# Kernel optimization log

Hardware: AMD Instinct MI355X
Metric: run time of the kernel (lower is better)

The kernel has to match this reference:

```python
import jax, jax.numpy as jnp
import numpy as np

B, S, D, H, HD = 1, 2048, 1024, 16, 64
WINDOW = 512
RADIUS = max(1, WINDOW // 2)
GLOBAL_IDX = (0, 1, 2, 3)
NEG = -1e9


def rotate_half(x):
    x1, x2 = jnp.split(x, 2, axis=-1)
    return jnp.concatenate([-x2, x1], axis=-1)


def apply_rope(x, cos, sin, pos):
    # x: [b, s, h, hd]; cos/sin: [max_pos, hd]; pos: [b, s]
    c = cos[pos][:, :, None, :]
    s_ = sin[pos][:, :, None, :]
    return x * c + rotate_half(x) * s_


def setup_inputs() -> dict:
    key = jax.random.key(0)
    ks = jax.random.split(key, 12)
    x = jax.random.normal(ks[0], (B, S, D), dtype=jnp.float32)
    # RoPE tables (standard construction)
    inv_freq = 1.0 / (10000.0 ** (jnp.arange(0, HD, 2, dtype=jnp.float32) / HD))
    t = jnp.arange(S, dtype=jnp.float32)
    freqs = jnp.outer(t, inv_freq)                      # [S, HD/2]
    emb = jnp.concatenate([freqs, freqs], axis=-1)      # [S, HD]
    cos_freqs = jnp.cos(emb)
    sin_freqs = jnp.sin(emb)
    position_ids = jnp.broadcast_to(jnp.arange(S, dtype=jnp.int32), (B, S))
    w = lambda k: jax.random.normal(k, (D, D), dtype=jnp.float32) * 0.02
    return {
        "x": x, "cos_freqs": cos_freqs, "sin_freqs": sin_freqs,
        "position_ids": position_ids,
        "Wqs": w(ks[1]), "Wks": w(ks[2]), "Wvs": w(ks[3]),
        "Wqg": w(ks[4]), "Wkg": w(ks[5]), "Wvg": w(ks[6]),
        "Wo": w(ks[7]),
    }


def reference(x, cos_freqs, sin_freqs, position_ids, Wqs, Wks, Wvs, Wqg, Wkg, Wvg, Wo):
    b, s, d = x.shape
    split = lambda y: y.reshape(b, s, H, HD)
    qs = split(x @ Wqs)
    ks_ = split(x @ Wks)
    vs = split(x @ Wvs)
    kg = split(x @ Wkg)
    vg = split(x @ Wvg)
    # (qg projection exists in the module but is unused by its forward math)
    qs = apply_rope(qs, cos_freqs, sin_freqs, position_ids)
    ks_ = apply_rope(ks_, cos_freqs, sin_freqs, position_ids)

    qs_t = jnp.swapaxes(qs, 1, 2)   # [b,h,s,hd]
    ks_t = jnp.swapaxes(ks_, 1, 2)
    vs_t = jnp.swapaxes(vs, 1, 2)
    scale = 1.0 / jnp.sqrt(jnp.float32(HD))

    # local sliding-window (causal) attention over dense scores
    scores = jnp.einsum('bhsd,bhtd->bhst', qs_t, ks_t) * scale
    i = jnp.arange(s)[:, None]
    j = jnp.arange(s)[None, :]
    mask = (jnp.abs(i - j) <= RADIUS) & (j <= i)
    scores = jnp.where(mask[None, None], scores, NEG)
    g = jnp.array(GLOBAL_IDX)
    scores = scores.at[:, :, :, g].add(1e9)  # same as per-index set(score+1e9)
    attn = jax.nn.softmax(scores, axis=-1)
    out_local = jnp.einsum('bhst,bhtd->bhsd', attn, vs_t)
    out_local = jnp.swapaxes(out_local, 1, 2).reshape(b, s, d)

    # global attention: all queries attend to the global-index columns of kg/vg
    kg_t = jnp.swapaxes(kg, 1, 2)
    vg_t = jnp.swapaxes(vg, 1, 2)
    scores_g = jnp.einsum('bhsd,bhtd->bhst', qs_t, kg_t) * scale
    col_mask = jnp.zeros((s,), dtype=bool).at[g].set(True)
    scores_g = jnp.where(col_mask[None, None, None, :], scores_g, NEG)
    attn_g = jax.nn.softmax(scores_g, axis=-1)
    out_global = jnp.einsum('bhst,bhtd->bhsd', attn_g, vg_t)
    out_global = jnp.swapaxes(out_global, 1, 2).reshape(b, s, d)

    return (out_local + out_global) @ Wo
```

## Files before the change

kernel.cpp:

```cpp
#include <hip/hip_runtime.h>

typedef _Float16 half8 __attribute__((ext_vector_type(8)));
typedef float floatx4 __attribute__((ext_vector_type(4)));

#define SEQ 2048
#define DMODEL 1024
#define NHEADS 16
#define HEADDIM 64
#define PW 5120

__global__ __launch_bounds__(256) void k_prep(
    const float* __restrict__ x,
    const float* __restrict__ w0, const float* __restrict__ w1, const float* __restrict__ w2,
    const float* __restrict__ w3, const float* __restrict__ w4, const float* __restrict__ w5,
    _Float16* __restrict__ xh, _Float16* __restrict__ wcat, _Float16* __restrict__ wot) {
  const int tid = threadIdx.x;
  const int b = blockIdx.x;
  if (b < 1024) {
    int base = b * 2048 + tid * 8;
    floatx4 f0 = *(const floatx4*)(x + base);
    floatx4 f1 = *(const floatx4*)(x + base + 4);
    half8 h;
    #pragma unroll
    for (int e = 0; e < 4; ++e) { h[e] = (_Float16)f0[e]; h[e + 4] = (_Float16)f1[e]; }
    *(half8*)(xh + base) = h;
    return;
  }
  __shared__ _Float16 T[64][72];
  int t = b - 1024;
  int z = t >> 8;
  int tile = t & 255;
  int k0 = (tile >> 4) * 64, n0 = (tile & 15) * 64;
  const float* W = (z == 0) ? w0 : (z == 1) ? w1 : (z == 2) ? w2
                 : (z == 3) ? w3 : (z == 4) ? w4 : w5;
  _Float16* dst = (z < 5) ? (wcat + (size_t)z * 1024 * 1024) : wot;

  int lr = tid >> 2, c0 = (tid & 3) * 16;
  #pragma unroll
  for (int i = 0; i < 4; ++i) {
    floatx4 f = *(const floatx4*)(W + (size_t)(k0 + lr) * DMODEL + n0 + c0 + i * 4);
    #pragma unroll
    for (int e = 0; e < 4; ++e) T[c0 + i * 4 + e][lr] = (_Float16)f[e];
  }
  __syncthreads();
  int nr = tid >> 2, s0 = (tid & 3) * 16;
  #pragma unroll
  for (int i = 0; i < 2; ++i) {
    half8 h = *(const half8*)&T[nr][s0 + i * 8];
    *(half8*)(dst + (size_t)(n0 + nr) * DMODEL + k0 + s0 + i * 8) = h;
  }
}

template <bool HALF_OUT, bool FUSE_ROPE>
__global__ __launch_bounds__(256) void k_gemm128(const _Float16* __restrict__ A,
                                                 const _Float16* __restrict__ Bt,
                                                 void* __restrict__ Cv,
                                                 const float* __restrict__ cos_t,
                                                 const float* __restrict__ sin_t,
                                                 const int* __restrict__ pos,
                                                 int M, int N, int K) {
  __shared__ _Float16 As[128][64];
  __shared__ _Float16 Bs[128][64];
  const int tid = threadIdx.x;
  const int lane = tid & 63;
  const int w = tid >> 6;
  const int wm = (w >> 1) * 64;
  const int wn = (w & 1) * 64;
  const int l15 = lane & 15;
  const int q4 = lane >> 4;
  const int m0 = blockIdx.x * 128;
  const int n0 = blockIdx.y * 128;

  floatx4 acc[4][4];
  #pragma unroll
  for (int i = 0; i < 4; ++i)
    #pragma unroll
    for (int j = 0; j < 4; ++j) acc[i][j] = (floatx4){0.f, 0.f, 0.f, 0.f};

  _Float16* asBase = &As[0][0];
  _Float16* bsBase = &Bs[0][0];
  const int swz = l15 & 7;

  for (int k0 = 0; k0 < K; k0 += 64) {
    __syncthreads();
    #pragma unroll
    for (int it = 0; it < 4; ++it) {
      int c = it * 256 + tid;
      int r = c >> 3, cc = c & 7;
      int g = cc ^ (r & 7);
      __builtin_amdgcn_global_load_lds(
          (const __attribute__((address_space(1))) void*)(A + (size_t)(m0 + r) * K + k0 + g * 8),
          (__attribute__((address_space(3))) void*)(asBase + (it * 256 + w * 64) * 8),
          16, 0, 0);
      __builtin_amdgcn_global_load_lds(
          (const __attribute__((address_space(1))) void*)(Bt + (size_t)(n0 + r) * K + k0 + g * 8),
          (__attribute__((address_space(3))) void*)(bsBase + (it * 256 + w * 64) * 8),
          16, 0, 0);
    }
    __syncthreads();

    #pragma unroll
    for (int kk = 0; kk < 2; ++kk) {
      int q = kk * 4 + q4;
      half8 af[4], bf[4];
      #pragma unroll
      for (int t = 0; t < 4; ++t) {
        int ar = wm + t * 16 + l15;
        af[t] = *(const half8*)(asBase + (size_t)ar * 64 + ((q ^ swz) * 8));
        int br = wn + t * 16 + l15;
        bf[t] = *(const half8*)(bsBase + (size_t)br * 64 + ((q ^ swz) * 8));
      }
      #pragma unroll
      for (int i = 0; i < 4; ++i)
        #pragma unroll
        for (int j = 0; j < 4; ++j)
          acc[i][j] = __builtin_amdgcn_mfma_f32_16x16x32_f16(af[i], bf[j], acc[i][j], 0, 0, 0);
    }
  }

  #pragma unroll
  for (int tm = 0; tm < 4; ++tm) {
    #pragma unroll
    for (int r = 0; r < 4; ++r) {
      int row = m0 + wm + tm * 16 + q4 * 4 + r;
      float v[4];
      #pragma unroll
      for (int tn = 0; tn < 4; ++tn) v[tn] = acc[tm][tn][r];
      if (FUSE_ROPE && n0 < 2048) {
        int p = pos[row];
        #pragma unroll
        for (int tn = 0; tn < 2; ++tn) {
          int d = tn * 16 + l15;
          float a = acc[tm][tn][r];
          float bvv = acc[tm][tn + 2][r];
          float c1 = cos_t[p * 64 + d],      s1 = sin_t[p * 64 + d];
          float c2 = cos_t[p * 64 + d + 32], s2 = sin_t[p * 64 + d + 32];
          v[tn]     = a * c1 - bvv * s1;
          v[tn + 2] = bvv * c2 + a * s2;
        }
      }
      #pragma unroll
      for (int tn = 0; tn < 4; ++tn) {
        int col = n0 + wn + tn * 16 + l15;
        if (HALF_OUT)
          ((_Float16*)Cv)[(size_t)row * N + col] = (_Float16)v[tn];
        else
          ((float*)Cv)[(size_t)row * N + col] = v[tn];
      }
    }
  }
}

template <bool HALF_OUT>
__global__ __launch_bounds__(256) void k_gemm(const _Float16* __restrict__ A,
                                              const _Float16* __restrict__ Bt,
                                              void* __restrict__ Cv, int M, int N, int K) {
  __shared__ _Float16 As[64][72];
  __shared__ _Float16 Bs[64][72];
  const int tid = threadIdx.x;
  const int lane = tid & 63;
  const int wave = tid >> 6;
  const int wm = (wave >> 1) * 32;
  const int wn = (wave & 1) * 32;
  const int row16 = lane & 15;
  const int q4 = lane >> 4;
  const int m0 = blockIdx.x * 64;
  const int n0 = blockIdx.y * 64;

  floatx4 acc[2][2];
  #pragma unroll
  for (int a = 0; a < 2; ++a)
    #pragma unroll
    for (int b = 0; b < 2; ++b) acc[a][b] = (floatx4){0.f, 0.f, 0.f, 0.f};

  for (int k0 = 0; k0 < K; k0 += 64) {
    __syncthreads();
    #pragma unroll
    for (int rep = 0; rep < 2; ++rep) {
      int c = tid + rep * 256;
      int r = c >> 3, q = c & 7;
      *(half8*)&As[r][q * 8] = *(const half8*)(A + (size_t)(m0 + r) * K + k0 + q * 8);
      *(half8*)&Bs[r][q * 8] = *(const half8*)(Bt + (size_t)(n0 + r) * K + k0 + q * 8);
    }
    __syncthreads();
    #pragma unroll
    for (int kk = 0; kk < 64; kk += 32) {
      half8 a0 = *(const half8*)&As[wm + row16][kk + q4 * 8];
      half8 a1 = *(const half8*)&As[wm + 16 + row16][kk + q4 * 8];
      half8 b0 = *(const half8*)&Bs[wn + row16][kk + q4 * 8];
      half8 b1 = *(const half8*)&Bs[wn + 16 + row16][kk + q4 * 8];
      acc[0][0] = __builtin_amdgcn_mfma_f32_16x16x32_f16(a0, b0, acc[0][0], 0, 0, 0);
      acc[0][1] = __builtin_amdgcn_mfma_f32_16x16x32_f16(a0, b1, acc[0][1], 0, 0, 0);
      acc[1][0] = __builtin_amdgcn_mfma_f32_16x16x32_f16(a1, b0, acc[1][0], 0, 0, 0);
      acc[1][1] = __builtin_amdgcn_mfma_f32_16x16x32_f16(a1, b1, acc[1][1], 0, 0, 0);
    }
  }
  #pragma unroll
  for (int im = 0; im < 2; ++im)
    #pragma unroll
    for (int in = 0; in < 2; ++in)
      #pragma unroll
      for (int r = 0; r < 4; ++r) {
        int row = m0 + wm + im * 16 + q4 * 4 + r;
        int col = n0 + wn + in * 16 + row16;
        if (HALF_OUT)
          ((_Float16*)Cv)[(size_t)row * N + col] = (_Float16)acc[im][in][r];
        else
          ((float*)Cv)[(size_t)row * N + col] = acc[im][in][r];
      }
}

__global__ __launch_bounds__(256, 4) void k_attn(const _Float16* __restrict__ proj,
                                                 _Float16* __restrict__ out) {
  const int tid = threadIdx.x;
  const int hb = blockIdx.y * 64;

  if (blockIdx.x >= 28) {
    const int i = (blockIdx.x - 28) * 4 + (tid >> 6);
    const int lane = tid & 63;
    const float scale = 0.125f;
    float qv = (float)proj[(size_t)i * PW + hb + lane];

    float sg[4];
    #pragma unroll
    for (int g = 0; g < 4; ++g) {
      float kgv = (float)proj[(size_t)g * PW + 3072 + hb + lane];
      float v = qv * kgv;
      #pragma unroll
      for (int off = 32; off; off >>= 1) v += __shfl_xor(v, off, 64);
      sg[g] = v * scale;
    }
    float mg = fmaxf(fmaxf(sg[0], sg[1]), fmaxf(sg[2], sg[3]));
    float dg = 0.f, og = 0.f;
    #pragma unroll
    for (int g = 0; g < 4; ++g) {
      float p = __expf(sg[g] - mg);
      dg += p;
      og += p * (float)proj[(size_t)g * PW + 4096 + hb + lane];
    }
    og /= dg;

    int jmin = (i >= 256) ? (i - 256) : 0;
    int jmax = (i < 3) ? i : 3;
    float acc = 0.f;
    for (int j = jmin; j <= jmax; ++j)
      acc += (float)proj[(size_t)j * PW + 2048 + hb + lane];
    float ol = acc / (float)(jmax - jmin + 1);

    out[(size_t)i * DMODEL + hb + lane] = (_Float16)(ol + og);
    return;
  }

  const int i0 = (blockIdx.x + 4) * 64;
  const int jlo = i0 - 256;
  const int lane = tid & 63;
  const int w = tid >> 6;
  const int l15 = lane & 15;
  const int q4 = lane >> 4;

  __shared__ _Float16 Qs[64][72];
  __shared__ _Float16 Kc[64][72];
  __shared__ _Float16 Vtc[64][72];
  __shared__ _Float16 Ps[64][72];
  __shared__ _Float16 kg_s[4][64];
  __shared__ _Float16 vg_s[4][64];
  __shared__ float svg_s[64];
  __shared__ float pg_s[4][64];

  #pragma unroll
  for (int rep = 0; rep < 2; ++rep) {
    int c = tid + rep * 256;
    int r = c >> 3, q = c & 7;
    *(half8*)&Qs[r][q * 8] = *(const half8*)(proj + (size_t)(i0 + r) * PW + hb + q * 8);
  }
  {
    int g = tid >> 6, c2 = tid & 63;
    kg_s[g][c2] = proj[(size_t)g * PW + 3072 + hb + c2];
    vg_s[g][c2] = proj[(size_t)g * PW + 4096 + hb + c2];
    if (tid < 64) {
      float s = 0.f;
      #pragma unroll
      for (int g2 = 0; g2 < 4; ++g2) s += (float)proj[(size_t)g2 * PW + 2048 + hb + tid];
      svg_s[tid] = s;
    }
  }
  __syncthreads();

  {
    int rid = lane >> 2, part = lane & 3;
    int ro = w * 16 + rid;
    float sg[4];
    #pragma unroll
    for (int g = 0; g < 4; ++g) {
      float acc = 0.f;
      #pragma unroll
      for (int u = 0; u < 16; ++u)
        acc += (float)Qs[ro][part * 16 + u] * (float)kg_s[g][part * 16 + u];
      acc += __shfl_xor(acc, 1, 64);
      acc += __shfl_xor(acc, 2, 64);
      sg[g] = acc * 0.125f;
    }
    float mg = fmaxf(fmaxf(sg[0], sg[1]), fmaxf(sg[2], sg[3]));
    float dg = 0.f;
    #pragma unroll
    for (int g = 0; g < 4; ++g) dg += __expf(sg[g] - mg);
    pg_s[part][ro] = __expf(sg[part] - mg) / dg;
  }

  half8 qf0 = *(const half8*)&Qs[w * 16 + l15][q4 * 8];
  half8 qf1 = *(const half8*)&Qs[w * 16 + l15][32 + q4 * 8];

  float m_r[4] = {0.f, 0.f, 0.f, 0.f};
  float l_r[4] = {4.f, 4.f, 4.f, 4.f};
  floatx4 oacc[4];
  #pragma unroll
  for (int cb = 0; cb < 4; ++cb) oacc[cb] = (floatx4){0.f, 0.f, 0.f, 0.f};

  for (int cc = 0; cc < 5; ++cc) {
    const int jbase = jlo + cc * 64;
    __syncthreads();
    #pragma unroll
    for (int rep = 0; rep < 2; ++rep) {
      int c = tid + rep * 256;
      int r = c >> 3, q = c & 7;
      *(half8*)&Kc[r][q * 8] =
          *(const half8*)(proj + (size_t)(jbase + r) * PW + 1024 + hb + q * 8);
    }
    #pragma unroll
    for (int it = 0; it < 2; ++it) {
      int idx = it * 256 + tid;
      int j = (idx & 7) + ((idx >> 6) << 3);
      int d0 = ((idx >> 3) & 7) * 8;
      half8 vv = *(const half8*)(proj + (size_t)(jbase + j) * PW + 2048 + hb + d0);
      #pragma unroll
      for (int u = 0; u < 8; ++u) Vtc[d0 + u][j] = vv[u];
    }
    __syncthreads();

    float sc[4][4];
    #pragma unroll
    for (int cb = 0; cb < 4; ++cb) {
      half8 b0 = *(const half8*)&Kc[cb * 16 + l15][q4 * 8];
      half8 b1 = *(const half8*)&Kc[cb * 16 + l15][32 + q4 * 8];
      floatx4 a = (floatx4){0.f, 0.f, 0.f, 0.f};
      a = __builtin_amdgcn_mfma_f32_16x16x32_f16(qf0, b0, a, 0, 0, 0);
      a = __builtin_amdgcn_mfma_f32_16x16x32_f16(qf1, b1, a, 0, 0, 0);
      #pragma unroll
      for (int r = 0; r < 4; ++r) sc[cb][r] = a[r];
    }

    #pragma unroll
    for (int r = 0; r < 4; ++r) {
      int ri = w * 16 + q4 * 4 + r;
      float rowmax = -1e30f;
      #pragma unroll
      for (int cb = 0; cb < 4; ++cb) {
        int jjg = cc * 64 + cb * 16 + l15;
        bool valid = (jjg >= ri) && (jjg <= ri + 256);
        float s = valid ? sc[cb][r] * 0.125f : -1e30f;
        sc[cb][r] = s;
        rowmax = fmaxf(rowmax, s);
      }
      #pragma unroll
      for (int off = 1; off < 16; off <<= 1)
        rowmax = fmaxf(rowmax, __shfl_xor(rowmax, off, 64));
      float m_new = fmaxf(m_r[r], rowmax);
      float alpha = __expf(m_r[r] - m_new);
      float rs = 0.f;
      #pragma unroll
      for (int cb = 0; cb < 4; ++cb) {
        float p = __expf(sc[cb][r] - m_new);
        Ps[w * 16 + q4 * 4 + r][cb * 16 + l15] = (_Float16)p;
        rs += p;
      }
      #pragma unroll
      for (int off = 1; off < 16; off <<= 1) rs += __shfl_xor(rs, off, 64);
      l_r[r] = l_r[r] * alpha + rs;
      m_r[r] = m_new;
      #pragma unroll
      for (int cb = 0; cb < 4; ++cb) oacc[cb][r] *= alpha;
    }

    half8 pf0 = *(const half8*)&Ps[w * 16 + l15][q4 * 8];
    half8 pf1 = *(const half8*)&Ps[w * 16 + l15][32 + q4 * 8];
    #pragma unroll
    for (int cb = 0; cb < 4; ++cb) {
      half8 v0 = *(const half8*)&Vtc[cb * 16 + l15][q4 * 8];
      half8 v1 = *(const half8*)&Vtc[cb * 16 + l15][32 + q4 * 8];
      oacc[cb] = __builtin_amdgcn_mfma_f32_16x16x32_f16(pf0, v0, oacc[cb], 0, 0, 0);
      oacc[cb] = __builtin_amdgcn_mfma_f32_16x16x32_f16(pf1, v1, oacc[cb], 0, 0, 0);
    }
  }

  #pragma unroll
  for (int r = 0; r < 4; ++r) {
    int ri = w * 16 + q4 * 4 + r;
    if (i0 + ri < 260) continue;
    float e0 = __expf(-m_r[r]);
    float inv = 1.f / l_r[r];
    #pragma unroll
    for (int cb = 0; cb < 4; ++cb) {
      int col = cb * 16 + l15;
      float ol = (oacc[cb][r] + e0 * svg_s[col]) * inv;
      float og = 0.f;
      #pragma unroll
      for (int g = 0; g < 4; ++g) og += pg_s[g][ri] * (float)vg_s[g][col];
      out[(size_t)(i0 + ri) * DMODEL + hb + col] = (_Float16)(ol + og);
    }
  }
}

extern "C" void kernel_launch(void* const* d_in, const int* in_sizes, int n_in,
                              void* d_out, int out_size, void* d_ws, size_t ws_size,
                              hipStream_t stream) {
  const float* x     = (const float*)d_in[0];
  const float* cos_t = (const float*)d_in[1];
  const float* sin_t = (const float*)d_in[2];
  const int*   pos   = (const int*)d_in[3];
  const float* Wqs   = (const float*)d_in[4];
  const float* Wks   = (const float*)d_in[5];
  const float* Wvs   = (const float*)d_in[6];
  const float* Wkg   = (const float*)d_in[8];
  const float* Wvg   = (const float*)d_in[9];
  const float* Wo    = (const float*)d_in[10];
  float* out = (float*)d_out;

  char* ws = (char*)d_ws;
  _Float16* xh   = (_Float16*)(ws);
  _Float16* wcat = (_Float16*)(ws + (4u << 20));
  _Float16* wot  = (_Float16*)(ws + (14u << 20));
  _Float16* proj = (_Float16*)(ws + (16u << 20));
  _Float16* attn = (_Float16*)(ws + (36u << 20));

  k_prep<<<2560, 256, 0, stream>>>(x, Wqs, Wks, Wvs, Wkg, Wvg, Wo, xh, wcat, wot);
  k_gemm128<true, true><<<dim3(SEQ / 128, PW / 128), 256, 0, stream>>>(
      xh, wcat, proj, cos_t, sin_t, pos, SEQ, PW, DMODEL);
  k_attn<<<dim3(93, NHEADS), 256, 0, stream>>>(proj, attn);
  k_gemm<false><<<dim3(SEQ / 64, DMODEL / 64), 256, 0, stream>>>(attn, wot, out, SEQ, DMODEL,
                                                                 DMODEL);
}
```

Measured before the change: 190.6 us.

## Deepen GEMM K-tile, split-K output GEMM, and double query rows per attention block

The 128x128 GEMM now stages 128-wide K slices, which halves the number of barrier iterations, and it gains a split-K mode. The output projection uses this mode with two K halves written to fp32 partial buffers, and a small reduce kernel sums them. This replaces the older 64x64-tile GEMM. The attention kernel processes 128 query rows per block, two 16-row groups per wave, so each K/V chunk is reused across more queries and fewer blocks are launched. The costs are double the LDS for the GEMM, which limits occupancy, extra fp32 partial traffic plus one more launch for the reduce, and higher register pressure in attention.

```diff
diff --git a/kernel.cpp b/kernel.cpp
--- a/kernel.cpp
+++ b/kernel.cpp
@@ -52,15 +52,13 @@
 }
 
 template <bool HALF_OUT, bool FUSE_ROPE>
-__global__ __launch_bounds__(256) void k_gemm128(const _Float16* __restrict__ A,
-                                                 const _Float16* __restrict__ Bt,
-                                                 void* __restrict__ Cv,
-                                                 const float* __restrict__ cos_t,
-                                                 const float* __restrict__ sin_t,
-                                                 const int* __restrict__ pos,
-                                                 int M, int N, int K) {
-  __shared__ _Float16 As[128][64];
-  __shared__ _Float16 Bs[128][64];
+__global__ __launch_bounds__(256, 2) void k_gemm128b(
+    const _Float16* __restrict__ A, const _Float16* __restrict__ Bt,
+    void* __restrict__ Cv, float* __restrict__ Cp0, float* __restrict__ Cp1,
+    const float* __restrict__ cos_t, const float* __restrict__ sin_t,
+    const int* __restrict__ pos, int M, int N, int K, int kLen) {
+  __shared__ _Float16 As[128][128];
+  __shared__ _Float16 Bs[128][128];
   const int tid = threadIdx.x;
   const int lane = tid & 63;
   const int w = tid >> 6;
@@ -70,6 +68,7 @@
   const int q4 = lane >> 4;
   const int m0 = blockIdx.x * 128;
   const int n0 = blockIdx.y * 128;
+  const int kStart = blockIdx.z * kLen;
 
   floatx4 acc[4][4];
   #pragma unroll
@@ -81,12 +80,12 @@
   _Float16* bsBase = &Bs[0][0];
   const int swz = l15 & 7;
 
-  for (int k0 = 0; k0 < K; k0 += 64) {
+  for (int k0 = kStart; k0 < kStart + kLen; k0 += 128) {
     __syncthreads();
     #pragma unroll
-    for (int it = 0; it < 4; ++it) {
+    for (int it = 0; it < 8; ++it) {
       int c = it * 256 + tid;
-      int r = c >> 3, cc = c & 7;
+      int r = c >> 4, cc = c & 15;
       int g = cc ^ (r & 7);
       __builtin_amdgcn_global_load_lds(
           (const __attribute__((address_space(1))) void*)(A + (size_t)(m0 + r) * K + k0 + g * 8),
@@ -100,15 +99,15 @@
     __syncthreads();
 
     #pragma unroll
-    for (int kk = 0; kk < 2; ++kk) {
+    for (int kk = 0; kk < 4; ++kk) {
       int q = kk * 4 + q4;
       half8 af[4], bf[4];
       #pragma unroll
       for (int t = 0; t < 4; ++t) {
         int ar = wm + t * 16 + l15;
-        af[t] = *(const half8*)(asBase + (size_t)ar * 64 + ((q ^ swz) * 8));
+        af[t] = *(const half8*)(asBase + (size_t)ar * 128 + ((q ^ swz) * 8));
         int br = wn + t * 16 + l15;
-        bf[t] = *(const half8*)(bsBase + (size_t)br * 64 + ((q ^ swz) * 8));
+        bf[t] = *(const half8*)(bsBase + (size_t)br * 128 + ((q ^ swz) * 8));
       }
       #pragma unroll
       for (int i = 0; i < 4; ++i)
@@ -118,6 +117,7 @@
     }
   }
 
+  float* P = HALF_OUT ? nullptr : (blockIdx.z ? Cp1 : Cp0);
   #pragma unroll
   for (int tm = 0; tm < 4; ++tm) {
     #pragma unroll
@@ -145,82 +145,31 @@
         if (HALF_OUT)
           ((_Float16*)Cv)[(size_t)row * N + col] = (_Float16)v[tn];
         else
-          ((float*)Cv)[(size_t)row * N + col] = v[tn];
+          P[(size_t)row * N + col] = v[tn];
       }
     }
   }
 }
 
-template <bool HALF_OUT>
-__global__ __launch_bounds__(256) void k_gemm(const _Float16* __restrict__ A,
-                                              const _Float16* __restrict__ Bt,
-                                              void* __restrict__ Cv, int M, int N, int K) {
-  __shared__ _Float16 As[64][72];
-  __shared__ _Float16 Bs[64][72];
-  const int tid = threadIdx.x;
-  const int lane = tid & 63;
-  const int wave = tid >> 6;
-  const int wm = (wave >> 1) * 32;
-  const int wn = (wave & 1) * 32;
-  const int row16 = lane & 15;
-  const int q4 = lane >> 4;
-  const int m0 = blockIdx.x * 64;
-  const int n0 = blockIdx.y * 64;
-
-  floatx4 acc[2][2];
-  #pragma unroll
-  for (int a = 0; a < 2; ++a)
-    #pragma unroll
-    for (int b = 0; b < 2; ++b) acc[a][b] = (floatx4){0.f, 0.f, 0.f, 0.f};
-
-  for (int k0 = 0; k0 < K; k0 += 64) {
-    __syncthreads();
-    #pragma unroll
-    for (int rep = 0; rep < 2; ++rep) {
-      int c = tid + rep * 256;
-      int r = c >> 3, q = c & 7;
-      *(half8*)&As[r][q * 8] = *(const half8*)(A + (size_t)(m0 + r) * K + k0 + q * 8);
-      *(half8*)&Bs[r][q * 8] = *(const half8*)(Bt + (size_t)(n0 + r) * K + k0 + q * 8);
-    }
-    __syncthreads();
-    #pragma unroll
-    for (int kk = 0; kk < 64; kk += 32) {
-      half8 a0 = *(const half8*)&As[wm + row16][kk + q4 * 8];
-      half8 a1 = *(const half8*)&As[wm + 16 + row16][kk + q4 * 8];
-      half8 b0 = *(const half8*)&Bs[wn + row16][kk + q4 * 8];
-      half8 b1 = *(const half8*)&Bs[wn + 16 + row16][kk + q4 * 8];
-      acc[0][0] = __builtin_amdgcn_mfma_f32_16x16x32_f16(a0, b0, acc[0][0], 0, 0, 0);
-      acc[0][1] = __builtin_amdgcn_mfma_f32_16x16x32_f16(a0, b1, acc[0][1], 0, 0, 0);
-      acc[1][0] = __builtin_amdgcn_mfma_f32_16x16x32_f16(a1, b0, acc[1][0], 0, 0, 0);
-      acc[1][1] = __builtin_amdgcn_mfma_f32_16x16x32_f16(a1, b1, acc[1][1], 0, 0, 0);
-    }
-  }
-  #pragma unroll
-  for (int im = 0; im < 2; ++im)
-    #pragma unroll
-    for (int in = 0; in < 2; ++in)
-      #pragma unroll
-      for (int r = 0; r < 4; ++r) {
-        int row = m0 + wm + im * 16 + q4 * 4 + r;
-        int col = n0 + wn + in * 16 + row16;
-        if (HALF_OUT)
-          ((_Float16*)Cv)[(size_t)row * N + col] = (_Float16)acc[im][in][r];
-        else
-          ((float*)Cv)[(size_t)row * N + col] = acc[im][in][r];
-      }
+__global__ __launch_bounds__(256) void k_reduce(const float* __restrict__ p0,
+                                                const float* __restrict__ p1,
+                                                float* __restrict__ out) {
+  int i = (blockIdx.x * 256 + threadIdx.x) * 4;
+  floatx4 a = *(const floatx4*)(p0 + i);
+  floatx4 b = *(const floatx4*)(p1 + i);
+  *(floatx4*)(out + i) = a + b;
 }
 
-__global__ __launch_bounds__(256, 4) void k_attn(const _Float16* __restrict__ proj,
+__global__ __launch_bounds__(256, 2) void k_attn(const _Float16* __restrict__ proj,
                                                  _Float16* __restrict__ out) {
   const int tid = threadIdx.x;
   const int hb = blockIdx.y * 64;
 
-  if (blockIdx.x >= 28) {
-    const int i = (blockIdx.x - 28) * 4 + (tid >> 6);
+  if (blockIdx.x >= 14) {
+    const int i = (blockIdx.x - 14) * 4 + (tid >> 6);
     const int lane = tid & 63;
     const float scale = 0.125f;
     float qv = (float)proj[(size_t)i * PW + hb + lane];
-
     float sg[4];
     #pragma unroll
     for (int g = 0; g < 4; ++g) {
@@ -239,36 +188,34 @@
       og += p * (float)proj[(size_t)g * PW + 4096 + hb + lane];
     }
     og /= dg;
-
     int jmin = (i >= 256) ? (i - 256) : 0;
     int jmax = (i < 3) ? i : 3;
     float acc = 0.f;
     for (int j = jmin; j <= jmax; ++j)
       acc += (float)proj[(size_t)j * PW + 2048 + hb + lane];
     float ol = acc / (float)(jmax - jmin + 1);
-
     out[(size_t)i * DMODEL + hb + lane] = (_Float16)(ol + og);
     return;
   }
 
-  const int i0 = (blockIdx.x + 4) * 64;
+  const int i0 = 256 + blockIdx.x * 128;
   const int jlo = i0 - 256;
   const int lane = tid & 63;
   const int w = tid >> 6;
   const int l15 = lane & 15;
   const int q4 = lane >> 4;
 
-  __shared__ _Float16 Qs[64][72];
+  __shared__ _Float16 Qs[128][72];
   __shared__ _Float16 Kc[64][72];
   __shared__ _Float16 Vtc[64][72];
-  __shared__ _Float16 Ps[64][72];
+  __shared__ _Float16 Ps[128][72];
   __shared__ _Float16 kg_s[4][64];
   __shared__ _Float16 vg_s[4][64];
   __shared__ float svg_s[64];
-  __shared__ float pg_s[4][64];
-
-  #pragma unroll
-  for (int rep = 0; rep < 2; ++rep) {
+  __shared__ float pg_s[4][128];
+
+  #pragma unroll
+  for (int rep = 0; rep < 4; ++rep) {
     int c = tid + rep * 256;
     int r = c >> 3, q = c & 7;
     *(half8*)&Qs[r][q * 8] = *(const half8*)(proj + (size_t)(i0 + r) * PW + hb + q * 8);
@@ -286,9 +233,10 @@
   }
   __syncthreads();
 
-  {
-    int rid = lane >> 2, part = lane & 3;
-    int ro = w * 16 + rid;
+  #pragma unroll
+  for (int pass = 0; pass < 2; ++pass) {
+    int ro = pass * 64 + w * 16 + (lane >> 2);
+    int part = lane & 3;
     float sg[4];
     #pragma unroll
     for (int g = 0; g < 4; ++g) {
@@ -307,16 +255,26 @@
     pg_s[part][ro] = __expf(sg[part] - mg) / dg;
   }
 
-  half8 qf0 = *(const half8*)&Qs[w * 16 + l15][q4 * 8];
-  half8 qf1 = *(const half8*)&Qs[w * 16 + l15][32 + q4 * 8];
-
-  float m_r[4] = {0.f, 0.f, 0.f, 0.f};
-  float l_r[4] = {4.f, 4.f, 4.f, 4.f};
-  floatx4 oacc[4];
-  #pragma unroll
-  for (int cb = 0; cb < 4; ++cb) oacc[cb] = (floatx4){0.f, 0.f, 0.f, 0.f};
-
-  for (int cc = 0; cc < 5; ++cc) {
+  half8 qf[2][2];
+  #pragma unroll
+  for (int rg = 0; rg < 2; ++rg) {
+    int row = w * 32 + rg * 16 + l15;
+    qf[rg][0] = *(const half8*)&Qs[row][q4 * 8];
+    qf[rg][1] = *(const half8*)&Qs[row][32 + q4 * 8];
+  }
+
+  float m_r[2][4], l_r[2][4];
+  floatx4 oacc[2][4];
+  #pragma unroll
+  for (int rg = 0; rg < 2; ++rg)
+    #pragma unroll
+    for (int cb = 0; cb < 4; ++cb) {
+      oacc[rg][cb] = (floatx4){0.f, 0.f, 0.f, 0.f};
+      m_r[rg][cb] = 0.f;
+      l_r[rg][cb] = 4.f;
+    }
+
+  for (int cc = 0; cc < 6; ++cc) {
     const int jbase = jlo + cc * 64;
     __syncthreads();
     #pragma unroll
@@ -337,77 +295,82 @@
     }
     __syncthreads();
 
-    float sc[4][4];
-    #pragma unroll
-    for (int cb = 0; cb < 4; ++cb) {
-      half8 b0 = *(const half8*)&Kc[cb * 16 + l15][q4 * 8];
-      half8 b1 = *(const half8*)&Kc[cb * 16 + l15][32 + q4 * 8];
-      floatx4 a = (floatx4){0.f, 0.f, 0.f, 0.f};
-      a = __builtin_amdgcn_mfma_f32_16x16x32_f16(qf0, b0, a, 0, 0, 0);
-      a = __builtin_amdgcn_mfma_f32_16x16x32_f16(qf1, b1, a, 0, 0, 0);
-      #pragma unroll
-      for (int r = 0; r < 4; ++r) sc[cb][r] = a[r];
-    }
-
+    #pragma unroll
+    for (int rg = 0; rg < 2; ++rg) {
+      float sc[4][4];
+      #pragma unroll
+      for (int cb = 0; cb < 4; ++cb) {
+        half8 b0 = *(const half8*)&Kc[cb * 16 + l15][q4 * 8];
+        half8 b1 = *(const half8*)&Kc[cb * 16 + l15][32 + q4 * 8];
+        floatx4 a = (floatx4){0.f, 0.f, 0.f, 0.f};
+        a = __builtin_amdgcn_mfma_f32_16x16x32_f16(qf[rg][0], b0, a, 0, 0, 0);
+        a = __builtin_amdgcn_mfma_f32_16x16x32_f16(qf[rg][1], b1, a, 0, 0, 0);
+        #pragma unroll
+        for (int r = 0; r < 4; ++r) sc[cb][r] = a[r];
+      }
+
+      #pragma unroll
+      for (int r = 0; r < 4; ++r) {
+        int ri = w * 32 + rg * 16 + q4 * 4 + r;
+        float rowmax = -1e30f;
+        #pragma unroll
+        for (int cb = 0; cb < 4; ++cb) {
+          int jjg = cc * 64 + cb * 16 + l15;
+          bool valid = (jjg >= ri) && (jjg <= ri + 256);
+          float s = valid ? sc[cb][r] * 0.125f : -1e30f;
+          sc[cb][r] = s;
+          rowmax = fmaxf(rowmax, s);
+        }
+        #pragma unroll
+        for (int off = 1; off < 16; off <<= 1)
+          rowmax = fmaxf(rowmax, __shfl_xor(rowmax, off, 64));
+        float m_new = fmaxf(m_r[rg][r], rowmax);
+        float alpha = __expf(m_r[rg][r] - m_new);
+        float rs = 0.f;
+        #pragma unroll
+        for (int cb = 0; cb < 4; ++cb) {
+          float p = __expf(sc[cb][r] - m_new);
+          Ps[ri][cb * 16 + l15] = (_Float16)p;
+          rs += p;
+        }
+        #pragma unroll
+        for (int off = 1; off < 16; off <<= 1) rs += __shfl_xor(rs, off, 64);
+        l_r[rg][r] = l_r[rg][r] * alpha + rs;
+        m_r[rg][r] = m_new;
+        #pragma unroll
+        for (int cb = 0; cb < 4; ++cb) oacc[rg][cb][r] *= alpha;
+      }
+
+      half8 pf0 = *(const half8*)&Ps[w * 32 + rg * 16 + l15][q4 * 8];
+      half8 pf1 = *(const half8*)&Ps[w * 32 + rg * 16 + l15][32 + q4 * 8];
+      #pragma unroll
+      for (int cb = 0; cb < 4; ++cb) {
+        half8 v0 = *(const half8*)&Vtc[cb * 16 + l15][q4 * 8];
+        half8 v1 = *(const half8*)&Vtc[cb * 16 + l15][32 + q4 * 8];
+        oacc[rg][cb] = __builtin_amdgcn_mfma_f32_16x16x32_f16(pf0, v0, oacc[rg][cb], 0, 0, 0);
+        oacc[rg][cb] = __builtin_amdgcn_mfma_f32_16x16x32_f16(pf1, v1, oacc[rg][cb], 0, 0, 0);
+      }
+    }
+  }
+
+  #pragma unroll
+  for (int rg = 0; rg < 2; ++rg)
     #pragma unroll
     for (int r = 0; r < 4; ++r) {
-      int ri = w * 16 + q4 * 4 + r;
-      float rowmax = -1e30f;
+      int ri = w * 32 + rg * 16 + q4 * 4 + r;
+      if (i0 + ri < 260) continue;
+      float e0 = __expf(-m_r[rg][r]);
+      float inv = 1.f / l_r[rg][r];
       #pragma unroll
       for (int cb = 0; cb < 4; ++cb) {
-        int jjg = cc * 64 + cb * 16 + l15;
-        bool valid = (jjg >= ri) && (jjg <= ri + 256);
-        float s = valid ? sc[cb][r] * 0.125f : -1e30f;
-        sc[cb][r] = s;
-        rowmax = fmaxf(rowmax, s);
-      }
-      #pragma unroll
-      for (int off = 1; off < 16; off <<= 1)
-        rowmax = fmaxf(rowmax, __shfl_xor(rowmax, off, 64));
-      float m_new = fmaxf(m_r[r], rowmax);
-      float alpha = __expf(m_r[r] - m_new);
-      float rs = 0.f;
-      #pragma unroll
-      for (int cb = 0; cb < 4; ++cb) {
-        float p = __expf(sc[cb][r] - m_new);
-        Ps[w * 16 + q4 * 4 + r][cb * 16 + l15] = (_Float16)p;
-        rs += p;
-      }
-      #pragma unroll
-      for (int off = 1; off < 16; off <<= 1) rs += __shfl_xor(rs, off, 64);
-      l_r[r] = l_r[r] * alpha + rs;
-      m_r[r] = m_new;
-      #pragma unroll
-      for (int cb = 0; cb < 4; ++cb) oacc[cb][r] *= alpha;
-    }
-
-    half8 pf0 = *(const half8*)&Ps[w * 16 + l15][q4 * 8];
-    half8 pf1 = *(const half8*)&Ps[w * 16 + l15][32 + q4 * 8];
-    #pragma unroll
-    for (int cb = 0; cb < 4; ++cb) {
-      half8 v0 = *(const half8*)&Vtc[cb * 16 + l15][q4 * 8];
-      half8 v1 = *(const half8*)&Vtc[cb * 16 + l15][32 + q4 * 8];
-      oacc[cb] = __builtin_amdgcn_mfma_f32_16x16x32_f16(pf0, v0, oacc[cb], 0, 0, 0);
-      oacc[cb] = __builtin_amdgcn_mfma_f32_16x16x32_f16(pf1, v1, oacc[cb], 0, 0, 0);
-    }
-  }
-
-  #pragma unroll
-  for (int r = 0; r < 4; ++r) {
-    int ri = w * 16 + q4 * 4 + r;
-    if (i0 + ri < 260) continue;
-    float e0 = __expf(-m_r[r]);
-    float inv = 1.f / l_r[r];
-    #pragma unroll
-    for (int cb = 0; cb < 4; ++cb) {
-      int col = cb * 16 + l15;
-      float ol = (oacc[cb][r] + e0 * svg_s[col]) * inv;
-      float og = 0.f;
-      #pragma unroll
-      for (int g = 0; g < 4; ++g) og += pg_s[g][ri] * (float)vg_s[g][col];
-      out[(size_t)(i0 + ri) * DMODEL + hb + col] = (_Float16)(ol + og);
-    }
-  }
+        int col = cb * 16 + l15;
+        float ol = (oacc[rg][cb][r] + e0 * svg_s[col]) * inv;
+        float og = 0.f;
+        #pragma unroll
+        for (int g = 0; g < 4; ++g) og += pg_s[g][ri] * (float)vg_s[g][col];
+        out[(size_t)(i0 + ri) * DMODEL + hb + col] = (_Float16)(ol + og);
+      }
+    }
 }
 
 extern "C" void kernel_launch(void* const* d_in, const int* in_sizes, int n_in,
@@ -431,11 +394,14 @@
   _Float16* wot  = (_Float16*)(ws + (14u << 20));
   _Float16* proj = (_Float16*)(ws + (16u << 20));
   _Float16* attn = (_Float16*)(ws + (36u << 20));
+  float* p0 = (float*)(ws);
+  float* p1 = (float*)(ws + (16u << 20));
 
   k_prep<<<2560, 256, 0, stream>>>(x, Wqs, Wks, Wvs, Wkg, Wvg, Wo, xh, wcat, wot);
-  k_gemm128<true, true><<<dim3(SEQ / 128, PW / 128), 256, 0, stream>>>(
-      xh, wcat, proj, cos_t, sin_t, pos, SEQ, PW, DMODEL);
-  k_attn<<<dim3(93, NHEADS), 256, 0, stream>>>(proj, attn);
-  k_gemm<false><<<dim3(SEQ / 64, DMODEL / 64), 256, 0, stream>>>(attn, wot, out, SEQ, DMODEL,
-                                                                 DMODEL);
+  k_gemm128b<true, true><<<dim3(16, 40, 1), 256, 0, stream>>>(
+      xh, wcat, proj, nullptr, nullptr, cos_t, sin_t, pos, SEQ, PW, DMODEL, DMODEL);
+  k_attn<<<dim3(79, NHEADS), 256, 0, stream>>>(proj, attn);
+  k_gemm128b<false, false><<<dim3(16, 8, 2), 256, 0, stream>>>(
+      attn, wot, nullptr, p0, p1, cos_t, sin_t, pos, SEQ, DMODEL, DMODEL, 512);
+  k_reduce<<<SEQ * DMODEL / 1024, 256, 0, stream>>>(p0, p1, out);
 }
```

Measured after the change: 183.8 us. 1.04x faster.
